# Kernel optimization log

Measured on AMD Instinct MI355X. Metric: run time of the kernel, lower is better.

The kernel has to match this reference:

```python
import jax, jax.numpy as jnp
import numpy as np

NBINS = 256  # skimage threshold_otsu default


def _minmax_norm(x):
    """Per-(image, band) min-max normalization over the last two (H, W) axes,
    mirroring FLIMAdaptiveDecoderLayer.normalize_by_band."""
    mn = x.min(axis=(-2, -1), keepdims=True)
    mx = x.max(axis=(-2, -1), keepdims=True)
    rng = mx - mn
    safe_rng = jnp.where(rng != 0.0, rng, 1.0)
    safe_mx = jnp.where(mx != 0.0, mx, 1.0)
    return jnp.where(rng != 0.0, (x - mn) / safe_rng,
                     jnp.where(mx != 0.0, (x - mn) / safe_mx, x))


def _otsu(x):
    """skimage.filters.threshold_otsu on a flat float array, 256 bins."""
    mn = x.min()
    mx = x.max()
    width = (mx - mn) / NBINS
    safe_w = jnp.where(width > 0.0, width, 1.0)
    idx = jnp.clip(jnp.floor((x - mn) / safe_w).astype(jnp.int32), 0, NBINS - 1)
    hist = jnp.zeros((NBINS,), dtype=x.dtype).at[idx].add(1.0)
    bc = mn + (jnp.arange(NBINS, dtype=x.dtype) + 0.5) * width  # bin centers
    w1 = jnp.cumsum(hist)
    w2 = jnp.cumsum(hist[::-1])[::-1]
    hb = hist * bc
    m1 = jnp.cumsum(hb) / jnp.maximum(w1, 1e-12)
    m2 = (jnp.cumsum(hb[::-1]) / jnp.maximum(jnp.cumsum(hist[::-1]), 1e-12))[::-1]
    var12 = w1[:-1] * w2[1:] * (m1[:-1] - m2[1:]) ** 2
    return bc[jnp.argmax(var12)]


def _forward(feature):
    B, C, H, W = feature.shape
    feat = _minmax_norm(feature)                                  # [B,C,H,W] in [0,1]
    # --- find_adaptive_threshold: Otsu over per-band means, variance of means ---
    means = feat.mean(axis=(-2, -1))                              # [B,C]
    thr = jax.vmap(_otsu)(means)                                  # [B]
    stdev = means.var(axis=1)                                     # means.std()**2 (ddof=0)
    low_end = jnp.where(thr > 0.1, thr - stdev, thr)              # [B]
    high_end = thr + stdev                                        # [B]
    # --- per-band Otsu + foreground proportion ---
    otsu_b = jax.vmap(_otsu)(feat.reshape(B * C, H * W)).reshape(B, C)
    pfg = (feat > otsu_b[:, :, None, None]).mean(axis=(-2, -1))   # [B,C]
    w = jnp.where((means >= high_end[:, None]) & (pfg > 0.2), -1.0,
                  jnp.where((means <= low_end[:, None]) & (pfg < 0.1), 1.0, 0.0))  # [B,C]
    # --- decode: F.conv2d(img[C,H,W], kernel[B,C,1,1]) per image -> [B,B,H,W] ---
    y = jnp.einsum('ichw,nc->inhw', feat, w) * 255.0
    y = jnp.maximum(y, 0.0)
    y = _minmax_norm(y)
    return y * 255.0


def setup_inputs() -> dict:
    key = jax.random.key(0)
    feature = jax.random.normal(key, (8, 64, 256, 256), dtype=jnp.float32)
    return {"feature": feature}


def reference(feature):
    return _forward(feature)
```

## Files before the change

### kernel.cpp

```cpp
#include <hip/hip_runtime.h>
#include <math.h>

#define HW_N 65536
#define NCH 64
#define NB 8
#define NBINS 256
#define NBAND 512

#define WS_MIN   0
#define WS_MAX   512
#define WS_SUM   1024
#define WS_PFG   2048
#define WS_MEANS 2560
#define WS_LO    3072
#define WS_HI    3080
#define WS_W     3088
#define WS_PMIN  3600
#define WS_PMAX  3664

__device__ int otsu_argmax(float* sh, float* shb, float* sv, int* si, int t) {
    for (int o = 1; o < NBINS; o <<= 1) {
        float a = 0.f, b = 0.f;
        if (t < NBINS) {
            a = sh[t]; b = shb[t];
            if (t >= o) { a += sh[t - o]; b += shb[t - o]; }
        }
        __syncthreads();
        if (t < NBINS) { sh[t] = a; shb[t] = b; }
        __syncthreads();
    }
    float N = sh[NBINS - 1], HB = shb[NBINS - 1];
    if (t < NBINS) {
        float v = -INFINITY;
        if (t < NBINS - 1) {
            float w1 = sh[t], w2 = N - w1;
            float m1 = shb[t] / fmaxf(w1, 1e-12f);
            float m2 = (HB - shb[t]) / fmaxf(w2, 1e-12f);
            float d = m1 - m2;
            v = (w1 * w2) * (d * d);
        }
        sv[t] = v; si[t] = t;
    }
    __syncthreads();
    for (int o = NBINS / 2; o; o >>= 1) {
        if (t < o) {
            float vo = sv[t + o]; int io = si[t + o];
            if (vo > sv[t] || (vo == sv[t] && io < si[t])) { sv[t] = vo; si[t] = io; }
        }
        __syncthreads();
    }
    return si[0];
}

__global__ __launch_bounds__(1024) void band_stats(const float* __restrict__ x,
                                                   float* __restrict__ ws) {
    int b = blockIdx.x;
    int t = threadIdx.x;
    const float4* p = (const float4*)(x + (size_t)b * HW_N);
    float mn = INFINITY, mx = -INFINITY, sum = 0.f;
#pragma unroll 4
    for (int k = t; k < HW_N / 4; k += 1024) {
        float4 v = p[k];
        mn = fminf(mn, fminf(fminf(v.x, v.y), fminf(v.z, v.w)));
        mx = fmaxf(mx, fmaxf(fmaxf(v.x, v.y), fmaxf(v.z, v.w)));
        sum += (v.x + v.y) + (v.z + v.w);
    }
    for (int o = 32; o; o >>= 1) {
        mn = fminf(mn, __shfl_down(mn, o));
        mx = fmaxf(mx, __shfl_down(mx, o));
        sum += __shfl_down(sum, o);
    }
    __shared__ float smn[16], smx[16], ssm[16];
    int wave = t >> 6, lane = t & 63;
    if (lane == 0) { smn[wave] = mn; smx[wave] = mx; ssm[wave] = sum; }
    __syncthreads();
    if (t == 0) {
        mn = smn[0]; mx = smx[0]; sum = ssm[0];
        for (int k = 1; k < 16; ++k) {
            mn = fminf(mn, smn[k]);
            mx = fmaxf(mx, smx[k]);
            sum += ssm[k];
        }
        ws[WS_MIN + b] = mn;
        ws[WS_MAX + b] = mx;
        ws[WS_SUM + b] = sum;
    }
}

__global__ __launch_bounds__(256) void image_otsu(float* __restrict__ ws) {
    int img = blockIdx.x;
    int t = threadIdx.x;
    __shared__ float sh[NBINS], shb[NBINS], sv[NBINS];
    __shared__ int si[NBINS];
    __shared__ float sred[4];

    float m = 0.f;
    if (t < NCH) {
        int b = img * NCH + t;
        float mn = ws[WS_MIN + b], mx = ws[WS_MAX + b], sum = ws[WS_SUM + b];
        float rng = mx - mn;
        m = (rng != 0.f) ? ((sum * (1.f / HW_N) - mn) / rng) : 0.f;
        ws[WS_MEANS + b] = m;
    }
    if (t < 64) {
        float mmn = m, mmx = m, msum = m;
        for (int o = 32; o; o >>= 1) {
            mmn = fminf(mmn, __shfl_down(mmn, o));
            mmx = fmaxf(mmx, __shfl_down(mmx, o));
            msum += __shfl_down(msum, o);
        }
        if (t == 0) { sred[0] = mmn; sred[1] = mmx; sred[2] = msum; }
    }
    if (t < NBINS) sh[t] = 0.f;
    __syncthreads();
    float mmn = sred[0], mmx = sred[1];
    float mbar = sred[2] * (1.f / NCH);
    if (t < 64) {
        float d = m - mbar;
        float sq = d * d;
        for (int o = 32; o; o >>= 1) sq += __shfl_down(sq, o);
        if (t == 0) sred[3] = sq * (1.f / NCH);
    }
    float rngm = mmx - mmn;
    float width = rngm * (1.f / NBINS);
    float safe_w = (width > 0.f) ? width : 1.f;
    if (t < 64) {
        int idx = (int)floorf((m - mmn) / safe_w);
        idx = min(max(idx, 0), NBINS - 1);
        atomicAdd(&sh[idx], 1.f);
    }
    __syncthreads();
    if (t < NBINS) shb[t] = sh[t] * (mmn + (t + 0.5f) * width);
    __syncthreads();
    int bi = otsu_argmax(sh, shb, sv, si, t);
    if (t == 0) {
        float var = sred[3];
        float thr = mmn + (bi + 0.5f) * width;
        ws[WS_LO + img] = (thr > 0.1f) ? (thr - var) : thr;
        ws[WS_HI + img] = thr + var;
    }
}

__global__ __launch_bounds__(1024) void band_otsu_pfg(const float* __restrict__ x,
                                                      float* __restrict__ ws) {
    int b = blockIdx.x;
    int t = threadIdx.x;
    float mn = ws[WS_MIN + b], mx = ws[WS_MAX + b];
    float rng = mx - mn;
    __shared__ unsigned ihist[NBINS], iabove[NBINS];
    __shared__ float sh[NBINS], shb[NBINS], sv[NBINS];
    __shared__ int si[NBINS];
    if (t < NBINS) { ihist[t] = 0u; iabove[t] = 0u; }
    __syncthreads();

    const float4* px = (const float4*)(x + (size_t)b * HW_N);
    if (rng != 0.f) {
        float inv256 = 256.f / rng;
#pragma unroll 4
        for (int k = t; k < HW_N / 4; k += 1024) {
            float4 v = px[k];
            float s0 = (v.x - mn) * inv256;
            float s1 = (v.y - mn) * inv256;
            float s2 = (v.z - mn) * inv256;
            float s3 = (v.w - mn) * inv256;
            int i0 = min((int)s0, NBINS - 1);
            int i1 = min((int)s1, NBINS - 1);
            int i2 = min((int)s2, NBINS - 1);
            int i3 = min((int)s3, NBINS - 1);
            atomicAdd(&ihist[i0], 1u);
            atomicAdd(&ihist[i1], 1u);
            atomicAdd(&ihist[i2], 1u);
            atomicAdd(&ihist[i3], 1u);
            if (s0 > i0 + 0.5f) atomicAdd(&iabove[i0], 1u);
            if (s1 > i1 + 0.5f) atomicAdd(&iabove[i1], 1u);
            if (s2 > i2 + 0.5f) atomicAdd(&iabove[i2], 1u);
            if (s3 > i3 + 0.5f) atomicAdd(&iabove[i3], 1u);
        }
    } else if (t == 0) {
        ihist[0] = HW_N;
    }
    __syncthreads();
    float width = (rng != 0.f) ? (1.f / NBINS) : 0.f;
    if (t < NBINS) {
        float h = (float)ihist[t];
        sh[t] = h;
        shb[t] = h * ((t + 0.5f) * width);
    }
    __syncthreads();
    int bi = otsu_argmax(sh, shb, sv, si, t);
    if (t == 0) {
        float N = sh[NBINS - 1];
        float cnt = (N - sh[bi]) + (float)iabove[bi];
        ws[WS_PFG + b] = cnt * (1.f / HW_N);
    }
}

__global__ __launch_bounds__(512) void compute_w(float* __restrict__ ws) {
    int t = threadIdx.x;
    int n = t >> 6;
    float m   = ws[WS_MEANS + t];
    float pfg = ws[WS_PFG + t];
    float lo  = ws[WS_LO + n];
    float hi  = ws[WS_HI + n];
    float wv = (m >= hi && pfg > 0.2f) ? -1.f
             : ((m <= lo && pfg < 0.1f) ? 1.f : 0.f);
    ws[WS_W + t] = wv;
    if (t < 64) {
        ws[WS_PMIN + t] = INFINITY;
        ws[WS_PMAX + t] = 0.f;
    }
}

__global__ __launch_bounds__(256, 2) void einsum_relu(const float* __restrict__ x,
                                                      float* __restrict__ ws,
                                                      float* __restrict__ out) {
    int img = blockIdx.x >> 6;
    int chunk = blockIdx.x & 63;
    int t = threadIdx.x;
    __shared__ float4 wt0[NCH], wt1[NCH];
    __shared__ float2 cp[NCH];
    if (t < NCH) {
        int b = img * NCH + t;
        float mn = ws[WS_MIN + b];
        float rng = ws[WS_MAX + b] - mn;
        cp[t] = make_float2(mn, (rng != 0.f) ? (1.f / rng) : 0.f);
        wt0[t] = make_float4(ws[WS_W + 0 * NCH + t], ws[WS_W + 1 * NCH + t],
                             ws[WS_W + 2 * NCH + t], ws[WS_W + 3 * NCH + t]);
        wt1[t] = make_float4(ws[WS_W + 4 * NCH + t], ws[WS_W + 5 * NCH + t],
                             ws[WS_W + 6 * NCH + t], ws[WS_W + 7 * NCH + t]);
    }
    __syncthreads();

    const int Q = HW_N / 4;
    int q = chunk * 256 + t;
    const float4* px = (const float4*)x + (size_t)img * NCH * Q + q;

    float4 acc0, acc1, acc2, acc3, acc4, acc5, acc6, acc7;
    acc0 = acc1 = acc2 = acc3 = acc4 = acc5 = acc6 = acc7 = make_float4(0.f, 0.f, 0.f, 0.f);

#define PROC(v, ci)                                                            \
    {                                                                          \
        float2 pc = cp[ci];                                                    \
        float4 w0 = wt0[ci], w1 = wt1[ci];                                     \
        float fx = (v.x - pc.x) * pc.y, fy = (v.y - pc.x) * pc.y;              \
        float fz = (v.z - pc.x) * pc.y, fw = (v.w - pc.x) * pc.y;              \
        acc0.x = fmaf(w0.x, fx, acc0.x); acc0.y = fmaf(w0.x, fy, acc0.y);      \
        acc0.z = fmaf(w0.x, fz, acc0.z); acc0.w = fmaf(w0.x, fw, acc0.w);      \
        acc1.x = fmaf(w0.y, fx, acc1.x); acc1.y = fmaf(w0.y, fy, acc1.y);      \
        acc1.z = fmaf(w0.y, fz, acc1.z); acc1.w = fmaf(w0.y, fw, acc1.w);      \
        acc2.x = fmaf(w0.z, fx, acc2.x); acc2.y = fmaf(w0.z, fy, acc2.y);      \
        acc2.z = fmaf(w0.z, fz, acc2.z); acc2.w = fmaf(w0.z, fw, acc2.w);      \
        acc3.x = fmaf(w0.w, fx, acc3.x); acc3.y = fmaf(w0.w, fy, acc3.y);      \
        acc3.z = fmaf(w0.w, fz, acc3.z); acc3.w = fmaf(w0.w, fw, acc3.w);      \
        acc4.x = fmaf(w1.x, fx, acc4.x); acc4.y = fmaf(w1.x, fy, acc4.y);      \
        acc4.z = fmaf(w1.x, fz, acc4.z); acc4.w = fmaf(w1.x, fw, acc4.w);      \
        acc5.x = fmaf(w1.y, fx, acc5.x); acc5.y = fmaf(w1.y, fy, acc5.y);      \
        acc5.z = fmaf(w1.y, fz, acc5.z); acc5.w = fmaf(w1.y, fw, acc5.w);      \
        acc6.x = fmaf(w1.z, fx, acc6.x); acc6.y = fmaf(w1.z, fy, acc6.y);      \
        acc6.z = fmaf(w1.z, fz, acc6.z); acc6.w = fmaf(w1.z, fw, acc6.w);      \
        acc7.x = fmaf(w1.w, fx, acc7.x); acc7.y = fmaf(w1.w, fy, acc7.y);      \
        acc7.z = fmaf(w1.w, fz, acc7.z); acc7.w = fmaf(w1.w, fw, acc7.w);      \
    }

#pragma unroll
    for (int c = 0; c < NCH; c += 4) {
        float4 v0 = px[(size_t)(c + 0) * Q];
        float4 v1 = px[(size_t)(c + 1) * Q];
        float4 v2 = px[(size_t)(c + 2) * Q];
        float4 v3 = px[(size_t)(c + 3) * Q];
        PROC(v0, c + 0)
        PROC(v1, c + 1)
        PROC(v2, c + 2)
        PROC(v3, c + 3)
    }
#undef PROC

    float4* out4 = (float4*)out + (size_t)img * NB * Q + q;
    float tmin[NB], tmax[NB];
    float4 accs[NB] = {acc0, acc1, acc2, acc3, acc4, acc5, acc6, acc7};
#pragma unroll
    for (int n = 0; n < NB; ++n) {
        float4 a = accs[n];
        float4 y;
        y.x = fmaxf(a.x * 255.f, 0.f);
        y.y = fmaxf(a.y * 255.f, 0.f);
        y.z = fmaxf(a.z * 255.f, 0.f);
        y.w = fmaxf(a.w * 255.f, 0.f);
        out4[(size_t)n * Q] = y;
        tmin[n] = fminf(fminf(y.x, y.y), fminf(y.z, y.w));
        tmax[n] = fmaxf(fmaxf(y.x, y.y), fmaxf(y.z, y.w));
    }
#pragma unroll
    for (int n = 0; n < NB; ++n) {
        for (int o = 32; o; o >>= 1) {
            tmin[n] = fminf(tmin[n], __shfl_down(tmin[n], o));
            tmax[n] = fmaxf(tmax[n], __shfl_down(tmax[n], o));
        }
    }
    if ((t & 63) == 0) {
#pragma unroll
        for (int n = 0; n < NB; ++n) {
            atomicMin((int*)&ws[WS_PMIN + img * NB + n], __float_as_int(tmin[n]));
            atomicMax((int*)&ws[WS_PMAX + img * NB + n], __float_as_int(tmax[n]));
        }
    }
}

__global__ __launch_bounds__(256) void norm_out(float* __restrict__ out,
                                                const float* __restrict__ ws) {
    int pair = blockIdx.x >> 4;
    int t = threadIdx.x;
    float mnp = ws[WS_PMIN + pair];
    float rng = ws[WS_PMAX + pair] - mnp;
    float4* p = (float4*)out + (size_t)pair * (HW_N / 4) + (size_t)(blockIdx.x & 15) * 1024;
    if (rng != 0.f) {
        float inv = 255.f / rng;
#pragma unroll
        for (int k = 0; k < 4; ++k) {
            float4 v = p[k * 256 + t];
            v.x = (v.x - mnp) * inv;
            v.y = (v.y - mnp) * inv;
            v.z = (v.z - mnp) * inv;
            v.w = (v.w - mnp) * inv;
            p[k * 256 + t] = v;
        }
    } else {
        float4 z = make_float4(0.f, 0.f, 0.f, 0.f);
#pragma unroll
        for (int k = 0; k < 4; ++k) p[k * 256 + t] = z;
    }
}

extern "C" void kernel_launch(void* const* d_in, const int* in_sizes, int n_in,
                              void* d_out, int out_size, void* d_ws, size_t ws_size,
                              hipStream_t stream) {
    const float* x = (const float*)d_in[0];
    float* out = (float*)d_out;
    float* ws = (float*)d_ws;
    band_stats<<<NBAND, 1024, 0, stream>>>(x, ws);
    image_otsu<<<NB, 256, 0, stream>>>(ws);
    band_otsu_pfg<<<NBAND, 1024, 0, stream>>>(x, ws);
    compute_w<<<1, 512, 0, stream>>>(ws);
    einsum_relu<<<NBAND, 256, 0, stream>>>(x, ws, out);
    norm_out<<<1024, 256, 0, stream>>>(out, ws);
}
```

Baseline: 325.9 us.

## Software-pipeline loads in three streaming kernels and pack histogram counters

New measurement: 347.3 us. 1.07x slower.

```diff
diff --git a/kernel.cpp b/kernel.cpp
--- a/kernel.cpp
+++ b/kernel.cpp
@@ -58,13 +58,31 @@
     int t = threadIdx.x;
     const float4* p = (const float4*)(x + (size_t)b * HW_N);
     float mn = INFINITY, mx = -INFINITY, sum = 0.f;
-#pragma unroll 4
-    for (int k = t; k < HW_N / 4; k += 1024) {
-        float4 v = p[k];
-        mn = fminf(mn, fminf(fminf(v.x, v.y), fminf(v.z, v.w)));
-        mx = fmaxf(mx, fmaxf(fmaxf(v.x, v.y), fmaxf(v.z, v.w)));
-        sum += (v.x + v.y) + (v.z + v.w);
-    }
+
+#define K1_RED(v)                                                              \
+    {                                                                          \
+        mn = fminf(mn, fminf(fminf(v.x, v.y), fminf(v.z, v.w)));               \
+        mx = fmaxf(mx, fmaxf(fmaxf(v.x, v.y), fmaxf(v.z, v.w)));               \
+        sum += (v.x + v.y) + (v.z + v.w);                                      \
+    }
+
+    float4 buf[4];
+#pragma unroll
+    for (int j = 0; j < 4; ++j) buf[j] = p[t + j * 1024];
+    for (int g = 1; g < 4; ++g) {
+        float4 nb[4];
+#pragma unroll
+        for (int j = 0; j < 4; ++j) nb[j] = p[t + (g * 4 + j) * 1024];
+        __builtin_amdgcn_sched_barrier(0);
+#pragma unroll
+        for (int j = 0; j < 4; ++j) K1_RED(buf[j]);
+#pragma unroll
+        for (int j = 0; j < 4; ++j) buf[j] = nb[j];
+    }
+#pragma unroll
+    for (int j = 0; j < 4; ++j) K1_RED(buf[j]);
+#undef K1_RED
+
     for (int o = 32; o; o >>= 1) {
         mn = fminf(mn, __shfl_down(mn, o));
         mx = fmaxf(mx, __shfl_down(mx, o));
@@ -147,42 +165,53 @@
     int t = threadIdx.x;
     float mn = ws[WS_MIN + b], mx = ws[WS_MAX + b];
     float rng = mx - mn;
-    __shared__ unsigned ihist[NBINS], iabove[NBINS];
+    __shared__ unsigned long long h64[NBINS];
     __shared__ float sh[NBINS], shb[NBINS], sv[NBINS];
     __shared__ int si[NBINS];
-    if (t < NBINS) { ihist[t] = 0u; iabove[t] = 0u; }
+    if (t < NBINS) h64[t] = 0ull;
     __syncthreads();
 
     const float4* px = (const float4*)(x + (size_t)b * HW_N);
     if (rng != 0.f) {
         float inv256 = 256.f / rng;
-#pragma unroll 4
-        for (int k = t; k < HW_N / 4; k += 1024) {
-            float4 v = px[k];
-            float s0 = (v.x - mn) * inv256;
-            float s1 = (v.y - mn) * inv256;
-            float s2 = (v.z - mn) * inv256;
-            float s3 = (v.w - mn) * inv256;
-            int i0 = min((int)s0, NBINS - 1);
-            int i1 = min((int)s1, NBINS - 1);
-            int i2 = min((int)s2, NBINS - 1);
-            int i3 = min((int)s3, NBINS - 1);
-            atomicAdd(&ihist[i0], 1u);
-            atomicAdd(&ihist[i1], 1u);
-            atomicAdd(&ihist[i2], 1u);
-            atomicAdd(&ihist[i3], 1u);
-            if (s0 > i0 + 0.5f) atomicAdd(&iabove[i0], 1u);
-            if (s1 > i1 + 0.5f) atomicAdd(&iabove[i1], 1u);
-            if (s2 > i2 + 0.5f) atomicAdd(&iabove[i2], 1u);
-            if (s3 > i3 + 0.5f) atomicAdd(&iabove[i3], 1u);
-        }
+#define K3_HIST(v)                                                             \
+    {                                                                          \
+        float s0 = (v.x - mn) * inv256;                                        \
+        float s1 = (v.y - mn) * inv256;                                        \
+        float s2 = (v.z - mn) * inv256;                                        \
+        float s3 = (v.w - mn) * inv256;                                        \
+        int i0 = min((int)s0, NBINS - 1);                                      \
+        int i1 = min((int)s1, NBINS - 1);                                      \
+        int i2 = min((int)s2, NBINS - 1);                                      \
+        int i3 = min((int)s3, NBINS - 1);                                      \
+        atomicAdd(&h64[i0], 1ull | ((unsigned long long)(s0 > i0 + 0.5f) << 32)); \
+        atomicAdd(&h64[i1], 1ull | ((unsigned long long)(s1 > i1 + 0.5f) << 32)); \
+        atomicAdd(&h64[i2], 1ull | ((unsigned long long)(s2 > i2 + 0.5f) << 32)); \
+        atomicAdd(&h64[i3], 1ull | ((unsigned long long)(s3 > i3 + 0.5f) << 32)); \
+    }
+        float4 buf[4];
+#pragma unroll
+        for (int j = 0; j < 4; ++j) buf[j] = px[t + j * 1024];
+        for (int g = 1; g < 4; ++g) {
+            float4 nb[4];
+#pragma unroll
+            for (int j = 0; j < 4; ++j) nb[j] = px[t + (g * 4 + j) * 1024];
+            __builtin_amdgcn_sched_barrier(0);
+#pragma unroll
+            for (int j = 0; j < 4; ++j) K3_HIST(buf[j]);
+#pragma unroll
+            for (int j = 0; j < 4; ++j) buf[j] = nb[j];
+        }
+#pragma unroll
+        for (int j = 0; j < 4; ++j) K3_HIST(buf[j]);
+#undef K3_HIST
     } else if (t == 0) {
-        ihist[0] = HW_N;
+        h64[0] = (unsigned long long)HW_N;
     }
     __syncthreads();
     float width = (rng != 0.f) ? (1.f / NBINS) : 0.f;
     if (t < NBINS) {
-        float h = (float)ihist[t];
+        float h = (float)(unsigned)(h64[t] & 0xffffffffull);
         sh[t] = h;
         shb[t] = h * ((t + 0.5f) * width);
     }
@@ -190,7 +219,8 @@
     int bi = otsu_argmax(sh, shb, sv, si, t);
     if (t == 0) {
         float N = sh[NBINS - 1];
-        float cnt = (N - sh[bi]) + (float)iabove[bi];
+        float above = (float)(unsigned)(h64[bi] >> 32);
+        float cnt = (N - sh[bi]) + above;
         ws[WS_PFG + b] = cnt * (1.f / HW_N);
     }
 }
@@ -211,9 +241,9 @@
     }
 }
 
-__global__ __launch_bounds__(256, 2) void einsum_relu(const float* __restrict__ x,
-                                                      float* __restrict__ ws,
-                                                      float* __restrict__ out) {
+__global__ __launch_bounds__(256) void einsum_relu(const float* __restrict__ x,
+                                                   float* __restrict__ ws,
+                                                   float* __restrict__ out) {
     int img = blockIdx.x >> 6;
     int chunk = blockIdx.x & 63;
     int t = threadIdx.x;
@@ -262,17 +292,21 @@
         acc7.z = fmaf(w1.w, fz, acc7.z); acc7.w = fmaf(w1.w, fw, acc7.w);      \
     }
 
-#pragma unroll
-    for (int c = 0; c < NCH; c += 4) {
-        float4 v0 = px[(size_t)(c + 0) * Q];
-        float4 v1 = px[(size_t)(c + 1) * Q];
-        float4 v2 = px[(size_t)(c + 2) * Q];
-        float4 v3 = px[(size_t)(c + 3) * Q];
-        PROC(v0, c + 0)
-        PROC(v1, c + 1)
-        PROC(v2, c + 2)
-        PROC(v3, c + 3)
-    }
+    float4 buf[16];
+#pragma unroll
+    for (int j = 0; j < 16; ++j) buf[j] = px[(size_t)j * Q];
+    for (int c = 0; c + 16 < NCH; c += 16) {
+        float4 nb[16];
+#pragma unroll
+        for (int j = 0; j < 16; ++j) nb[j] = px[(size_t)(c + 16 + j) * Q];
+        __builtin_amdgcn_sched_barrier(0);
+#pragma unroll
+        for (int j = 0; j < 16; ++j) PROC(buf[j], c + j);
+#pragma unroll
+        for (int j = 0; j < 16; ++j) buf[j] = nb[j];
+    }
+#pragma unroll
+    for (int j = 0; j < 16; ++j) PROC(buf[j], 48 + j);
 #undef PROC
 
     float4* out4 = (float4*)out + (size_t)img * NB * Q + q;
@@ -341,6 +375,6 @@
     image_otsu<<<NB, 256, 0, stream>>>(ws);
     band_otsu_pfg<<<NBAND, 1024, 0, stream>>>(x, ws);
     compute_w<<<1, 512, 0, stream>>>(ws);
-    einsum_relu<<<NBAND, 256, 0, stream>>>(x, ws, out);
+    einsum_relu<<<512, 256, 0, stream>>>(x, ws, out);
     norm_out<<<1024, 256, 0, stream>>>(out, ws);
 }
```
